# Kernel optimization log

Hardware: AMD Instinct MI355X
Metric: run time of the kernel (lower is better)

The kernel has to match this reference:

```python
import jax, jax.numpy as jnp
import numpy as np

N, E = 50000, 1_600_000
IN, HID, OUT = 2048, 64, 64


def setup_inputs() -> dict:
    key = jax.random.key(0)
    k1, k2, k3, k4 = jax.random.split(key, 4)
    x = jax.random.normal(k1, (N, IN), dtype=jnp.float32)
    edge_index = jax.random.randint(k2, (2, E), 0, N, dtype=jnp.int64)
    W1 = jax.random.normal(k3, (IN, HID), dtype=jnp.float32) / np.sqrt(IN)
    b1 = jnp.zeros((HID,), dtype=jnp.float32)
    W2 = jax.random.normal(k4, (HID, OUT), dtype=jnp.float32) / np.sqrt(HID)
    b2 = jnp.zeros((OUT,), dtype=jnp.float32)
    return {"x": x, "edge_index": edge_index, "W1": W1, "b1": b1, "W2": W2, "b2": b2}


def gcn_conv(x, edge_index, W, b):
    # PyG GCNConv: h = XW; out = D^{-1/2} (A + I) D^{-1/2} h + b
    n = x.shape[0]
    h = x @ W  # [n, d_out]
    loops = jnp.arange(n, dtype=edge_index.dtype)
    src = jnp.concatenate([edge_index[0], loops])  # [E+n]
    dst = jnp.concatenate([edge_index[1], loops])
    deg = jax.ops.segment_sum(jnp.ones_like(dst, dtype=h.dtype), dst, num_segments=n)
    dinv = jax.lax.rsqrt(deg)  # deg >= 1 because of self-loops
    norm = dinv[src] * dinv[dst]  # [E+n]
    out = jax.ops.segment_sum(h[src] * norm[:, None], dst, num_segments=n)
    return out + b


def reference(x, edge_index, W1, b1, W2, b2):
    h = jax.nn.relu(gcn_conv(x, edge_index, W1, b1))
    h = jax.nn.relu(gcn_conv(h, edge_index, W2, b2))
    return h.mean(axis=0)  # [OUT]
```

## Files before the change

### kernel.cpp

```cpp
#include <hip/hip_runtime.h>
#include <hip/hip_bf16.h>

typedef __attribute__((ext_vector_type(8))) short short8_t;
typedef __attribute__((ext_vector_type(4))) float f32x4;

__device__ __forceinline__ short f2bf(float x){
  union { float f; unsigned u; } v; v.f = x;
  unsigned r = v.u + 0x7fffu + ((v.u >> 16) & 1u);
  return (short)(r >> 16);
}
__device__ __forceinline__ unsigned pack2(float lo, float hi){
  return (unsigned)(unsigned short)f2bf(lo) | ((unsigned)(unsigned short)f2bf(hi) << 16);
}
__device__ __forceinline__ float bf2f(unsigned short u){
  union { unsigned u; float f; } v; v.u = ((unsigned)u) << 16; return v.f;
}

__global__ __launch_bounds__(256) void k_wconv2(const float* __restrict__ W1, short* __restrict__ Wb1,
                                                const float* __restrict__ W2, short* __restrict__ Wb2){
  int tid = blockIdx.x*256 + threadIdx.x;
  const float* W; short* Wb; int t;
  if (tid < 64*2048){ W = W1; Wb = Wb1; t = tid; }
  else if (tid < 64*2048 + 2*2048){ W = W2; Wb = Wb2; t = tid - 64*2048; }
  else return;
  int e  = t & 7;
  int l  = (t >> 3) & 63;
  int nt = (t >> 9) & 3;
  int kt = t >> 11;
  int k  = kt*32 + (l >> 4)*8 + e;
  int col = nt*16 + (l & 15);
  Wb[t] = f2bf(W[(size_t)k*64 + col]);
}

__global__ __launch_bounds__(256, 4) void k_gemm1_hist(const float* __restrict__ A, const short* __restrict__ Wb,
                                                       unsigned short* __restrict__ h1, int M,
                                                       const int* __restrict__ ei, int* __restrict__ cnt16,
                                                       int* __restrict__ rank, int E, int N){
  __shared__ unsigned short lds[64*256];
  int b = blockIdx.x, tid = threadIdx.x;
  int wid = tid >> 6, lane = tid & 63;
  int row0 = b*64 + wid*16;
  int rfrag = lane & 15, grp = lane >> 4;
  char* ldsb = (char*)lds;
  const short8_t* wb = (const short8_t*)Wb + lane;
  f32x4 acc0 = {0.f,0.f,0.f,0.f}, acc1 = acc0, acc2 = acc0, acc3 = acc0;

  int wbase = wid*16*512;
  int wsel  = (lane >> 1);
  int whalf = (lane & 1) << 3;

  const float* rowp[16];
  #pragma unroll
  for (int r = 0; r < 16; ++r){
    int rowc = row0 + r; if (rowc >= M) rowc = M - 1;
    rowp[r] = A + (size_t)rowc*2048 + lane*4;
  }

  for (int ko = 0; ko < 8; ++ko){
    float4 fv[8];
    #pragma unroll
    for (int r = 0; r < 8; ++r) fv[r] = *(const float4*)(rowp[r] + ko*256);
    #pragma unroll
    for (int r = 0; r < 8; ++r){
      uint2 p; p.x = pack2(fv[r].x, fv[r].y); p.y = pack2(fv[r].z, fv[r].w);
      *(uint2*)(ldsb + wbase + r*512 + ((wsel ^ (r & 7)) << 4) + whalf) = p;
    }
    #pragma unroll
    for (int r = 0; r < 8; ++r) fv[r] = *(const float4*)(rowp[8 + r] + ko*256);
    #pragma unroll
    for (int r = 0; r < 8; ++r){
      uint2 p; p.x = pack2(fv[r].x, fv[r].y); p.y = pack2(fv[r].z, fv[r].w);
      *(uint2*)(ldsb + wbase + (8 + r)*512 + ((wsel ^ ((8 + r) & 7)) << 4) + whalf) = p;
    }
    asm volatile("s_waitcnt lgkmcnt(0)" ::: "memory");
    #pragma unroll
    for (int kt = 0; kt < 8; ++kt){
      short8_t af = *(const short8_t*)(ldsb + wbase + rfrag*512 + ((((kt<<2) + grp) ^ (rfrag & 7)) << 4));
      int ktg = ko*8 + kt;
      short8_t b0 = wb[(ktg*4+0)*64];
      short8_t b1 = wb[(ktg*4+1)*64];
      short8_t b2 = wb[(ktg*4+2)*64];
      short8_t b3 = wb[(ktg*4+3)*64];
      acc0 = __builtin_amdgcn_mfma_f32_16x16x32_bf16(af, b0, acc0, 0,0,0);
      acc1 = __builtin_amdgcn_mfma_f32_16x16x32_bf16(af, b1, acc1, 0,0,0);
      acc2 = __builtin_amdgcn_mfma_f32_16x16x32_bf16(af, b2, acc2, 0,0,0);
      acc3 = __builtin_amdgcn_mfma_f32_16x16x32_bf16(af, b3, acc3, 0,0,0);
    }
  }

  int orow = row0 + grp*4;
  unsigned short* op = h1 + (size_t)orow*64 + rfrag;
  #pragma unroll
  for (int reg = 0; reg < 4; ++reg){
    if (orow + reg < M){
      op[reg*64 +  0] = (unsigned short)f2bf(acc0[reg]);
      op[reg*64 + 16] = (unsigned short)f2bf(acc1[reg]);
      op[reg*64 + 32] = (unsigned short)f2bf(acc2[reg]);
      op[reg*64 + 48] = (unsigned short)f2bf(acc3[reg]);
    }
  }

  int lo = b << 11, hi = lo + 2048; if (hi > E) hi = E;
  int* cs = cnt16 + (size_t)(b & 15)*N;
  for (int i = lo + tid; i < hi; i += 256)
    rank[i] = atomicAdd(&cs[ei[E + i]], 1);
}

__global__ __launch_bounds__(256) void k_part(const int* __restrict__ cnt16, int* __restrict__ partial, int N){
  int b = blockIdx.x, t = threadIdx.x;
  int chunk = (N + 255) >> 8;
  int lo = b*chunk, hi = lo + chunk; if (hi > N) hi = N;
  int s = 0;
  for (int i = lo + t; i < hi; i += 256){
    #pragma unroll
    for (int sh = 0; sh < 16; ++sh) s += cnt16[(size_t)sh*N + i];
  }
  __shared__ int sm[256];
  sm[t] = s; __syncthreads();
  for (int d = 128; d; d >>= 1){ if (t < d) sm[t] += sm[t+d]; __syncthreads(); }
  if (t == 0) partial[b] = sm[0];
}

__global__ __launch_bounds__(256) void k_scan2(const int* __restrict__ cnt16, const int* __restrict__ partial,
                                               int* __restrict__ off, int* __restrict__ sbase,
                                               float* __restrict__ dinv, int N){
  int b = blockIdx.x, t = threadIdx.x;
  __shared__ int ps[256];
  ps[t] = partial[t]; __syncthreads();
  for (int d = 1; d < 256; d <<= 1){
    int v = (t >= d) ? ps[t-d] : 0; __syncthreads(); ps[t] += v; __syncthreads();
  }
  int base  = b ? ps[b-1] : 0;
  int total = ps[255];
  int chunk = (N + 255) >> 8;
  int lo = b*chunk, hi = lo + chunk; if (hi > N) hi = N;
  __shared__ int vs[256];
  int run = base;
  for (int j0 = lo; j0 < hi; j0 += 256){
    int i = j0 + t;
    int cs[16]; int c = 0;
    if (i < hi){
      #pragma unroll
      for (int sh = 0; sh < 16; ++sh){ cs[sh] = cnt16[(size_t)sh*N + i]; c += cs[sh]; }
    }
    vs[t] = (i < hi) ? c : 0; __syncthreads();
    for (int d = 1; d < 256; d <<= 1){
      int v = (t >= d) ? vs[t-d] : 0; __syncthreads(); vs[t] += v; __syncthreads();
    }
    if (i < hi){
      int excl = run + vs[t] - c;
      off[i] = excl;
      dinv[i] = rsqrtf((float)(c + 1));
      int runs = excl;
      #pragma unroll
      for (int sh = 0; sh < 16; ++sh){ sbase[(size_t)sh*N + i] = runs; runs += cs[sh]; }
    }
    run += vs[255];
    __syncthreads();
  }
  if (b == 255 && t == 0) off[N] = total;
}

__global__ __launch_bounds__(256) void k_scatter(const int* __restrict__ ei, const int* __restrict__ sbase,
                                                 const int* __restrict__ rank, int* __restrict__ ebuf,
                                                 int E, int N){
  int i = blockIdx.x*256 + threadIdx.x;
  if (i < E){
    int s = ei[i], d = ei[E + i];
    int sh = (i >> 11) & 15;
    ebuf[sbase[(size_t)sh*N + d] + rank[i]] = s;
  }
}

template<int KTILES>
__global__ __launch_bounds__(256) void k_gemm_sm(const unsigned short* __restrict__ Ah,
                                                 const short* __restrict__ Wb,
                                                 unsigned short* __restrict__ out, int M, int lda){
  int wid = threadIdx.x >> 6, lane = threadIdx.x & 63;
  int row0 = (blockIdx.x*4 + wid)*16;
  if (row0 >= M) return;
  int r = lane & 15, g = lane >> 4;
  const short8_t* wb = (const short8_t*)Wb + lane;
  f32x4 acc0 = {0.f,0.f,0.f,0.f}, acc1 = acc0, acc2 = acc0, acc3 = acc0;
  #pragma unroll
  for (int kt = 0; kt < KTILES; ++kt){
    short8_t af = *(const short8_t*)(Ah + (size_t)(row0 + r)*lda + kt*32 + g*8);
    short8_t b0 = wb[(kt*4+0)*64];
    short8_t b1 = wb[(kt*4+1)*64];
    short8_t b2 = wb[(kt*4+2)*64];
    short8_t b3 = wb[(kt*4+3)*64];
    acc0 = __builtin_amdgcn_mfma_f32_16x16x32_bf16(af, b0, acc0, 0,0,0);
    acc1 = __builtin_amdgcn_mfma_f32_16x16x32_bf16(af, b1, acc1, 0,0,0);
    acc2 = __builtin_amdgcn_mfma_f32_16x16x32_bf16(af, b2, acc2, 0,0,0);
    acc3 = __builtin_amdgcn_mfma_f32_16x16x32_bf16(af, b3, acc3, 0,0,0);
  }
  int orow = row0 + g*4;
  unsigned short* op = out + (size_t)orow*64 + r;
  #pragma unroll
  for (int reg = 0; reg < 4; ++reg){
    if (orow + reg < M){
      op[reg*64 +  0] = (unsigned short)f2bf(acc0[reg]);
      op[reg*64 + 16] = (unsigned short)f2bf(acc1[reg]);
      op[reg*64 + 32] = (unsigned short)f2bf(acc2[reg]);
      op[reg*64 + 48] = (unsigned short)f2bf(acc3[reg]);
    }
  }
}

template<bool FUSE>
__global__ __launch_bounds__(256) void k_agg(const unsigned short* __restrict__ hin, const int* __restrict__ off,
                                             const int* __restrict__ ebuf, const float* __restrict__ dinv,
                                             const float* __restrict__ bias, void* __restrict__ outp, int N){
  int lane = threadIdx.x & 63, wid = threadIdx.x >> 6;
  float b = bias[lane];
  float fsum = 0.f;
  int stride = gridDim.x*4;
  for (int i = blockIdx.x*4 + wid; i < N; i += stride){
    float di = dinv[i];
    float acc = di*bf2f(hin[(size_t)i*64 + lane]);
    int j  = off[i];
    int j1 = off[i+1];
    for (; j + 8 <= j1; j += 8){
      int s0 = ebuf[j],   s1 = ebuf[j+1], s2 = ebuf[j+2], s3 = ebuf[j+3];
      int s4 = ebuf[j+4], s5 = ebuf[j+5], s6 = ebuf[j+6], s7 = ebuf[j+7];
      float w0 = dinv[s0], w1 = dinv[s1], w2 = dinv[s2], w3 = dinv[s3];
      float w4 = dinv[s4], w5 = dinv[s5], w6 = dinv[s6], w7 = dinv[s7];
      float h0 = bf2f(hin[(size_t)s0*64 + lane]);
      float h1v = bf2f(hin[(size_t)s1*64 + lane]);
      float h2 = bf2f(hin[(size_t)s2*64 + lane]);
      float h3 = bf2f(hin[(size_t)s3*64 + lane]);
      float h4 = bf2f(hin[(size_t)s4*64 + lane]);
      float h5 = bf2f(hin[(size_t)s5*64 + lane]);
      float h6 = bf2f(hin[(size_t)s6*64 + lane]);
      float h7 = bf2f(hin[(size_t)s7*64 + lane]);
      acc += w0*h0 + w1*h1v + w2*h2 + w3*h3 + w4*h4 + w5*h5 + w6*h6 + w7*h7;
    }
    for (; j < j1; ++j){
      int s = ebuf[j];
      acc += dinv[s]*bf2f(hin[(size_t)s*64 + lane]);
    }
    float z = fmaxf(di*acc + b, 0.f);
    if (FUSE) fsum += z;
    else ((unsigned short*)outp)[(size_t)i*64 + lane] = (unsigned short)f2bf(z);
  }
  if (FUSE){
    __shared__ float sm[4][64];
    sm[wid][lane] = fsum;
    __syncthreads();
    if (wid == 0)
      ((float*)outp)[(size_t)blockIdx.x*64 + lane] = sm[0][lane] + sm[1][lane] + sm[2][lane] + sm[3][lane];
  }
}

__global__ __launch_bounds__(256) void k_final(const float* __restrict__ part, float* __restrict__ out,
                                               int NB, float invN){
  int f = blockIdx.x;
  float s = 0.f;
  for (int b = threadIdx.x; b < NB; b += 256) s += part[(size_t)b*64 + f];
  __shared__ float sm[256];
  sm[threadIdx.x] = s; __syncthreads();
  for (int d = 128; d > 0; d >>= 1){
    if (threadIdx.x < d) sm[threadIdx.x] += sm[threadIdx.x + d];
    __syncthreads();
  }
  if (threadIdx.x == 0) out[f] = sm[0]*invN;
}

extern "C" void kernel_launch(void* const* d_in, const int* in_sizes, int n_in,
                              void* d_out, int out_size, void* d_ws, size_t ws_size,
                              hipStream_t stream){
  const float* x  = (const float*)d_in[0];
  const int*   ei = (const int*)d_in[1];
  const float* W1 = (const float*)d_in[2];
  const float* b1 = (const float*)d_in[3];
  const float* W2 = (const float*)d_in[4];
  const float* b2 = (const float*)d_in[5];
  float* out = (float*)d_out;

  const int IN = 2048;
  int N = in_sizes[0] / IN;
  int E = in_sizes[1] / 2;

  char* w = (char*)d_ws;
  auto alloc = [&](size_t bytes){ char* p = w; w += (bytes + 255) & ~255ULL; return (void*)p; };
  int*   cnt16   = (int*)  alloc((size_t)16*N*4);
  int*   off     = (int*)  alloc((size_t)(N+1)*4);
  int*   sbase   = (int*)  alloc((size_t)16*N*4);
  float* dinv    = (float*)alloc((size_t)N*4);
  int*   partial = (int*)  alloc(256*4);
  int*   rank    = (int*)  alloc((size_t)E*4);
  int*   ebuf    = (int*)  alloc((size_t)E*4);
  short* Wb1     = (short*)alloc((size_t)64*2048*2);
  short* Wb2     = (short*)alloc((size_t)2*2048*2);
  unsigned short* h1 = (unsigned short*)alloc((size_t)N*64*2);
  unsigned short* z1 = (unsigned short*)alloc((size_t)N*64*2);
  const int NB2 = 2048;
  float* part    = (float*)alloc((size_t)NB2*64*4);

  int EB = (E + 255)/256;
  int GB = (N + 63)/64;
  int smblocks = ((N + 15)/16 + 3)/4;

  hipMemsetAsync(cnt16, 0, (size_t)16*N*4, stream);
  k_wconv2 <<<(64*2048 + 2*2048 + 255)/256, 256, 0, stream>>>(W1, Wb1, W2, Wb2);
  k_gemm1_hist<<<GB, 256, 0, stream>>>(x, Wb1, h1, N, ei, cnt16, rank, E, N);
  k_part   <<<256, 256, 0, stream>>>(cnt16, partial, N);
  k_scan2  <<<256, 256, 0, stream>>>(cnt16, partial, off, sbase, dinv, N);
  k_scatter<<<EB, 256, 0, stream>>>(ei, sbase, rank, ebuf, E, N);
  k_agg<false><<<NB2, 256, 0, stream>>>(h1, off, ebuf, dinv, b1, (void*)z1, N);
  k_gemm_sm<2><<<smblocks, 256, 0, stream>>>(z1, Wb2, h1, N, 64);
  k_agg<true> <<<NB2, 256, 0, stream>>>(h1, off, ebuf, dinv, b2, (void*)part, N);
  k_final  <<<64, 256, 0, stream>>>(part, out, NB2, 1.0f/(float)N);
}
```

Baseline: 347.7 us.

## Stage fp32 A tiles via global_load_lds and convert to bf16 with cvt_pk

Replaces the register round-trip (global load to VGPRs, software bf16 pack, LDS store) in the first GEMM with direct global-to-LDS DMA loads of the raw fp32 rows into padded per-wave LDS buffers. The bf16 conversion moves to the LDS read side and uses the hardware v_cvt_pk_bf16_f32 instruction instead of the manual rounding code. The goal is to cut VGPR pressure and ALU work in this memory-bound GEMM. In exchange, LDS use doubles because tiles are held in fp32, the occupancy hint in launch_bounds is dropped, and there is still no prefetch overlap because each stage waits on vmcnt(0).

```diff
diff --git a/kernel.cpp b/kernel.cpp
--- a/kernel.cpp
+++ b/kernel.cpp
@@ -9,11 +9,15 @@
   unsigned r = v.u + 0x7fffu + ((v.u >> 16) & 1u);
   return (short)(r >> 16);
 }
-__device__ __forceinline__ unsigned pack2(float lo, float hi){
-  return (unsigned)(unsigned short)f2bf(lo) | ((unsigned)(unsigned short)f2bf(hi) << 16);
-}
 __device__ __forceinline__ float bf2f(unsigned short u){
   union { unsigned u; float f; } v; v.u = ((unsigned)u) << 16; return v.f;
+}
+__device__ __forceinline__ unsigned cvtpk(float lo, float hi){
+  unsigned r; asm("v_cvt_pk_bf16_f32 %0, %1, %2" : "=v"(r) : "v"(lo), "v"(hi)); return r;
+}
+__device__ __forceinline__ void gll16(const float* g, void* l){
+  __builtin_amdgcn_global_load_lds((const __attribute__((address_space(1))) char*)g,
+                                   (__attribute__((address_space(3))) char*)l, 16, 0, 0);
 }
 
 __global__ __launch_bounds__(256) void k_wconv2(const float* __restrict__ W1, short* __restrict__ Wb1,
@@ -32,59 +36,50 @@
   Wb[t] = f2bf(W[(size_t)k*64 + col]);
 }
 
-__global__ __launch_bounds__(256, 4) void k_gemm1_hist(const float* __restrict__ A, const short* __restrict__ Wb,
-                                                       unsigned short* __restrict__ h1, int M,
-                                                       const int* __restrict__ ei, int* __restrict__ cnt16,
-                                                       int* __restrict__ rank, int E, int N){
-  __shared__ unsigned short lds[64*256];
+__global__ __launch_bounds__(256) void k_gemm1_hist(const float* __restrict__ A, const short* __restrict__ Wb,
+                                                    unsigned short* __restrict__ h1, int M,
+                                                    const int* __restrict__ ei, int* __restrict__ cnt16,
+                                                    int* __restrict__ rank, int E, int N){
+  __shared__ char lds[4*16*1040];
   int b = blockIdx.x, tid = threadIdx.x;
   int wid = tid >> 6, lane = tid & 63;
   int row0 = b*64 + wid*16;
   int rfrag = lane & 15, grp = lane >> 4;
-  char* ldsb = (char*)lds;
+  char* wls = lds + wid*16*1040;
   const short8_t* wb = (const short8_t*)Wb + lane;
   f32x4 acc0 = {0.f,0.f,0.f,0.f}, acc1 = acc0, acc2 = acc0, acc3 = acc0;
 
-  int wbase = wid*16*512;
-  int wsel  = (lane >> 1);
-  int whalf = (lane & 1) << 3;
-
-  const float* rowp[16];
+  int rowc[16];
   #pragma unroll
   for (int r = 0; r < 16; ++r){
-    int rowc = row0 + r; if (rowc >= M) rowc = M - 1;
-    rowp[r] = A + (size_t)rowc*2048 + lane*4;
+    int rc = row0 + r; rowc[r] = (rc < M) ? rc : (M - 1);
   }
 
   for (int ko = 0; ko < 8; ++ko){
-    float4 fv[8];
     #pragma unroll
-    for (int r = 0; r < 8; ++r) fv[r] = *(const float4*)(rowp[r] + ko*256);
-    #pragma unroll
-    for (int r = 0; r < 8; ++r){
-      uint2 p; p.x = pack2(fv[r].x, fv[r].y); p.y = pack2(fv[r].z, fv[r].w);
-      *(uint2*)(ldsb + wbase + r*512 + ((wsel ^ (r & 7)) << 4) + whalf) = p;
-    }
-    #pragma unroll
-    for (int r = 0; r < 8; ++r) fv[r] = *(const float4*)(rowp[8 + r] + ko*256);
-    #pragma unroll
-    for (int r = 0; r < 8; ++r){
-      uint2 p; p.x = pack2(fv[r].x, fv[r].y); p.y = pack2(fv[r].z, fv[r].w);
-      *(uint2*)(ldsb + wbase + (8 + r)*512 + ((wsel ^ ((8 + r) & 7)) << 4) + whalf) = p;
-    }
-    asm volatile("s_waitcnt lgkmcnt(0)" ::: "memory");
+    for (int r = 0; r < 16; ++r)
+      gll16(A + (size_t)rowc[r]*2048 + ko*256 + lane*4, wls + r*1040);
+    asm volatile("s_waitcnt vmcnt(0)" ::: "memory");
+    __builtin_amdgcn_sched_barrier(0);
     #pragma unroll
     for (int kt = 0; kt < 8; ++kt){
-      short8_t af = *(const short8_t*)(ldsb + wbase + rfrag*512 + ((((kt<<2) + grp) ^ (rfrag & 7)) << 4));
+      const float* fp = (const float*)(wls + rfrag*1040 + (kt*32 + grp*8)*4);
+      float4 a0 = *(const float4*)fp;
+      float4 a1 = *(const float4*)(fp + 4);
+      union { unsigned u[4]; short8_t s; } af;
+      af.u[0] = cvtpk(a0.x, a0.y);
+      af.u[1] = cvtpk(a0.z, a0.w);
+      af.u[2] = cvtpk(a1.x, a1.y);
+      af.u[3] = cvtpk(a1.z, a1.w);
       int ktg = ko*8 + kt;
       short8_t b0 = wb[(ktg*4+0)*64];
       short8_t b1 = wb[(ktg*4+1)*64];
       short8_t b2 = wb[(ktg*4+2)*64];
       short8_t b3 = wb[(ktg*4+3)*64];
-      acc0 = __builtin_amdgcn_mfma_f32_16x16x32_bf16(af, b0, acc0, 0,0,0);
-      acc1 = __builtin_amdgcn_mfma_f32_16x16x32_bf16(af, b1, acc1, 0,0,0);
-      acc2 = __builtin_amdgcn_mfma_f32_16x16x32_bf16(af, b2, acc2, 0,0,0);
-      acc3 = __builtin_amdgcn_mfma_f32_16x16x32_bf16(af, b3, acc3, 0,0,0);
+      acc0 = __builtin_amdgcn_mfma_f32_16x16x32_bf16(af.s, b0, acc0, 0,0,0);
+      acc1 = __builtin_amdgcn_mfma_f32_16x16x32_bf16(af.s, b1, acc1, 0,0,0);
+      acc2 = __builtin_amdgcn_mfma_f32_16x16x32_bf16(af.s, b2, acc2, 0,0,0);
+      acc3 = __builtin_amdgcn_mfma_f32_16x16x32_bf16(af.s, b3, acc3, 0,0,0);
     }
   }
 
```

Result: faster. 321.6 us (median of 2 runs) (-7.5%).
